# Performance work log

Hardware: AMD Instinct MI355X
Metric: run time of the kernel (lower is better)

## Reference

```python
import jax, jax.numpy as jnp
import numpy as np

DIM = 768
NUM_HEADS = 12
HEAD_DIM = DIM // NUM_HEADS
SCALE = HEAD_DIM ** -0.5


def setup_inputs() -> dict:
    key = jax.random.key(0)
    k1, k2, k3, k4 = jax.random.split(key, 4)
    x = jax.random.normal(k1, (4, 2048, DIM), dtype=jnp.float32)
    # Linear weights stored as [in, out] (torch stores [out, in]; math identical)
    w_qkv = jax.random.normal(k2, (DIM, 3 * DIM), dtype=jnp.float32) * (DIM ** -0.5)
    w_proj = jax.random.normal(k3, (DIM, DIM), dtype=jnp.float32) * (DIM ** -0.5)
    b_proj = jax.random.normal(k4, (DIM,), dtype=jnp.float32) * 0.02
    return {"x": x, "w_qkv": w_qkv, "w_proj": w_proj, "b_proj": b_proj}


def reference(x, w_qkv, w_proj, b_proj):
    b, n, d = x.shape
    qkv = x @ w_qkv  # [b, n, 3*d]
    # '(qkv h d)' layout: leading split is qkv, then heads, then head_dim
    qkv = qkv.reshape(b, n, 3, NUM_HEADS, HEAD_DIM).transpose(2, 0, 3, 1, 4)
    q, k, v = qkv[0], qkv[1], qkv[2]  # each [b, h, n, hd]
    alpha = jnp.einsum('bhqd,bhkd->bhqk', q, k) * SCALE  # [b, h, n, n]
    attn = jax.nn.softmax(alpha, axis=-1)
    out = jnp.einsum('bhqk,bhkd->bhqd', attn, v)  # [b, h, n, hd]
    out = out.transpose(0, 2, 1, 3).reshape(b, n, d)  # b n (h d)
    return out @ w_proj + b_proj
```

## Files before the change

### kernel.cpp

```cpp
#include <hip/hip_runtime.h>
#include <hip/hip_bf16.h>


typedef short s16x8 __attribute__((ext_vector_type(8)));
typedef short s16x4 __attribute__((ext_vector_type(4)));
typedef float f32x4 __attribute__((ext_vector_type(4)));
typedef float f32x16 __attribute__((ext_vector_type(16)));
typedef unsigned int u32;
typedef unsigned int u32x2 __attribute__((ext_vector_type(2)));
typedef unsigned int u32x4 __attribute__((ext_vector_type(4)));

#define NHEADS 12
#define HDIM   64
#define SEQ    2048
#define BATCH  4
#define DMODEL 768
#define MTOT   (BATCH*SEQ)
#define K3     (3*DMODEL)
#define QSCALE 0.18033688f

#define CAST_BLOCKS ((MTOT * DMODEL / 4) / 256)
#define TQ_BLOCKS   ((K3 / 64) * (DMODEL / 64))
#define TP_BLOCKS   ((DMODEL / 64) * (DMODEL / 64))

__device__ __forceinline__ short f2bf(float f) {
  return __builtin_bit_cast(short, __float2bfloat16(f));
}
__device__ __forceinline__ u32 pack2bf_rh(float lo, float hi) {
  u32 a = __builtin_bit_cast(u32, lo) + 0x8000u;
  u32 b = __builtin_bit_cast(u32, hi) + 0x8000u;
  return __builtin_amdgcn_perm(b, a, 0x07060302u);
}
__device__ __forceinline__ u32 pack2bf_tr(float lo, float hi) {
  return __builtin_amdgcn_perm(__builtin_bit_cast(u32, hi),
                               __builtin_bit_cast(u32, lo), 0x07060302u);
}
__device__ __forceinline__ f32x4 mfma16(s16x8 a, s16x8 b, f32x4 c) {
  return __builtin_amdgcn_mfma_f32_16x16x32_bf16(a, b, c, 0, 0, 0);
}
__device__ __forceinline__ f32x16 mfma32(s16x8 a, s16x8 b, f32x16 c) {
  return __builtin_amdgcn_mfma_f32_32x32x16_bf16(a, b, c, 0, 0, 0);
}
__device__ __forceinline__ void gload_lds16(const void* g, void* l) {
  __builtin_amdgcn_global_load_lds(
      (const __attribute__((address_space(1))) void*)g,
      (__attribute__((address_space(3))) void*)l, 16, 0, 0);
}

__global__ __launch_bounds__(256) void k_prep(const float* __restrict__ x,
                                              const float* __restrict__ w_qkv,
                                              const float* __restrict__ w_proj,
                                              short* __restrict__ Xb,
                                              short* __restrict__ WqkvT,
                                              short* __restrict__ WprojT) {
  __shared__ short t[64][74];
  const int bid = blockIdx.x, tid = threadIdx.x;

  if (bid < CAST_BLOCKS) {
    int i = bid * 256 + tid;
    float4 f = reinterpret_cast<const float4*>(x)[i];
    s16x4 v;
    v[0] = f2bf(f.x); v[1] = f2bf(f.y); v[2] = f2bf(f.z); v[3] = f2bf(f.w);
    reinterpret_cast<s16x4*>(Xb)[i] = v;
    return;
  }
  const float* in;
  short* out;
  int C, idx;
  if (bid < CAST_BLOCKS + TQ_BLOCKS) {
    in = w_qkv; out = WqkvT; C = K3; idx = bid - CAST_BLOCKS;
  } else {
    in = w_proj; out = WprojT; C = DMODEL; idx = bid - CAST_BLOCKS - TQ_BLOCKS;
  }
  const int c0 = (idx % (C / 64)) * 64;
  const int r0 = (idx / (C / 64)) * 64;
  {
    const int r = tid >> 2, j0 = (tid & 3) * 16;
    const float* ip = in + (size_t)(r0 + r) * C + c0 + j0;
#pragma unroll
    for (int k = 0; k < 16; k += 4) {
      float4 f = *reinterpret_cast<const float4*>(ip + k);
      t[r][j0 + k + 0] = f2bf(f.x); t[r][j0 + k + 1] = f2bf(f.y);
      t[r][j0 + k + 2] = f2bf(f.z); t[r][j0 + k + 3] = f2bf(f.w);
    }
  }
  __syncthreads();
  {
    const int c = tid >> 2, rr0 = (tid & 3) * 16;
    short* op = out + (size_t)(c0 + c) * DMODEL + r0 + rr0;
#pragma unroll
    for (int k = 0; k < 16; k += 8) {
      s16x8 v;
#pragma unroll
      for (int q = 0; q < 8; ++q) v[q] = t[rr0 + k + q][c];
      *reinterpret_cast<s16x8*>(op + k) = v;
    }
  }
}

__global__ __launch_bounds__(512, 4) void k_gemm_qkv(const short* __restrict__ Xb,
                                                     const short* __restrict__ WT,
                                                     short* __restrict__ Qb,
                                                     short* __restrict__ Kb,
                                                     short* __restrict__ Vt) {
  __shared__ short As[2][64 * 64];
  __shared__ short Bs[2][128 * 64];
  const int tid = threadIdx.x;
  const int orig = blockIdx.x;
  const int wg = (orig & 7) * (2304 / 8) + (orig >> 3);
  const int n0 = (wg % 18) * 128, m0 = (wg / 18) * 64;
  const int lane = tid & 63, w = tid >> 6;
  const int wr = w >> 2, wc = w & 3;
  const int g = lane >> 4, r16 = lane & 15;

  const int srow = tid >> 3;
  const int scc  = (tid & 7) ^ (srow & 7);
  const short* gaA = Xb + (size_t)(m0 + srow) * DMODEL + scc * 8;
  const short* gaB = WT + (size_t)(n0 + srow) * DMODEL + scc * 8;
  short* lA = &As[0][0] + w * 512;
  short* lB = &Bs[0][0] + w * 512;

#define GSTAGE(b, k0)                                                          \
  { gload_lds16(gaA + (k0),                         lA + (b) * 4096);          \
    gload_lds16(gaB + (k0),                         lB + (b) * 8192);          \
    gload_lds16(gaB + (size_t)64 * DMODEL + (k0),   lB + (b) * 8192 + 4096); }

  f32x4 acc[2][2] = {};
  const int key = (r16 & 7) << 4;

  GSTAGE(0, 0)
  for (int t = 0; t < DMODEL / 64; ++t) {
    const int b = t & 1;
    if (t + 1 < DMODEL / 64) {
      GSTAGE(b ^ 1, (t + 1) * 64)
      asm volatile("s_waitcnt vmcnt(3)" ::: "memory");
    } else {
      asm volatile("s_waitcnt vmcnt(0)" ::: "memory");
    }
    __builtin_amdgcn_s_barrier();
    __builtin_amdgcn_sched_barrier(0);

    const char* Ab = (const char*)&As[0][0] + b * 8192;
    const char* Bb = (const char*)&Bs[0][0] + b * 16384;
    s16x8 a[2][2], bf[2][2];
#pragma unroll
    for (int i = 0; i < 2; ++i)
#pragma unroll
      for (int kk = 0; kk < 2; ++kk)
        a[i][kk] = *(const s16x8*)(Ab + (((wr * 32 + i * 16 + r16) * 128 + kk * 64 + g * 16) ^ key));
#pragma unroll
    for (int j = 0; j < 2; ++j)
#pragma unroll
      for (int kk = 0; kk < 2; ++kk)
        bf[j][kk] = *(const s16x8*)(Bb + (((wc * 32 + j * 16 + r16) * 128 + kk * 64 + g * 16) ^ key));
#pragma unroll
    for (int kk = 0; kk < 2; ++kk)
#pragma unroll
      for (int i = 0; i < 2; ++i)
#pragma unroll
        for (int j = 0; j < 2; ++j)
          acc[i][j] = mfma16(a[i][kk], bf[j][kk], acc[i][j]);

    __builtin_amdgcn_sched_barrier(0);
    __builtin_amdgcn_s_barrier();
  }
#undef GSTAGE

#pragma unroll
  for (int i = 0; i < 2; ++i) {
#pragma unroll
    for (int jn = 0; jn < 2; ++jn) {
      const int c = n0 + wc * 32 + jn * 16 + r16;
#pragma unroll
      for (int rr = 0; rr < 4; ++rr) {
        const int m = m0 + wr * 32 + i * 16 + g * 4 + rr;
        const float a = acc[i][jn][rr];
        const int bb = m >> 11, ns = m & 2047;
        if (c < DMODEL) {
          const int h = c >> 6, d = c & 63;
          Qb[((bb * NHEADS + h) * SEQ + ns) * HDIM + d] = f2bf(a * QSCALE);
        } else if (c < 2 * DMODEL) {
          const int cc = c - DMODEL, h = cc >> 6, d = cc & 63;
          Kb[((bb * NHEADS + h) * SEQ + ns) * HDIM + d] = f2bf(a);
        } else {
          const int cc = c - 2 * DMODEL, h = cc >> 6, d = cc & 63;
          Vt[((bb * NHEADS + h) * HDIM + d) * SEQ + ns] = f2bf(a);
        }
      }
    }
  }
}

__global__ __launch_bounds__(256, 3) void k_attn(const short* __restrict__ Qb,
                                                 const short* __restrict__ Kb,
                                                 const short* __restrict__ Vtg,
                                                 short* __restrict__ Ctx) {
  __shared__ short Kt[3][64 * 64];
  __shared__ short Vt[3][64 * 64];

  const int tid = threadIdx.x, lane = tid & 63, w = tid >> 6;
  const int l31 = lane & 31, hi = lane >> 5;

  const int orig = blockIdx.y * gridDim.x + blockIdx.x;
  const int wg = (orig & 7) * (768 / 8) + (orig >> 3);
  const int qx = wg & 15;
  const int bh = wg >> 4;
  const int bb = bh / NHEADS, h = bh - bb * NHEADS;
  const int q0w = qx * 128 + w * 32;

  const short* Qp = Qb + (size_t)bh * SEQ * HDIM;
  const short* Kp = Kb + (size_t)bh * SEQ * HDIM;
  const short* Vp = Vtg + (size_t)bh * HDIM * SEQ;
  const int key4 = (lane & 7) << 4;

  const int sr1 = tid >> 3, sr2 = 32 + sr1;
  const int c1 = (tid & 7) ^ (sr1 & 7);
  const int c2 = (tid & 7) ^ (sr2 & 7);
  const short* kg1 = Kp + sr1 * HDIM + c1 * 8;
  const short* kg2 = Kp + sr2 * HDIM + c2 * 8;
  const short* vg1 = Vp + (size_t)sr1 * SEQ + c1 * 8;
  const short* vg2 = Vp + (size_t)sr2 * SEQ + c2 * 8;
  short* kld = &Kt[0][0] + w * 512;
  short* vld = &Vt[0][0] + w * 512;

#define STAGE(b, kb)                                                           \
  { gload_lds16(kg1 + (size_t)(kb) * HDIM, kld + (b) * 4096);                  \
    gload_lds16(kg2 + (size_t)(kb) * HDIM, kld + (b) * 4096 + 2048);           \
    gload_lds16(vg1 + (kb),                vld + (b) * 4096);                  \
    gload_lds16(vg2 + (kb),                vld + (b) * 4096 + 2048); }

  s16x8 aq[4];
#pragma unroll
  for (int kk = 0; kk < 4; ++kk)
    aq[kk] = *reinterpret_cast<const s16x8*>(&Qp[(q0w + l31) * HDIM + kk * 16 + hi * 8]);

  float sacc = 0.f;
  f32x16 accO[2] = {};

  STAGE(0, 0)
  int cur = 0, nxt = 1;

  for (int t = 0; t < SEQ / 64; ++t) {
    if (t + 1 < SEQ / 64) {
      STAGE(nxt, (t + 1) * 64)
      asm volatile("s_waitcnt vmcnt(4)" ::: "memory");
    } else {
      asm volatile("s_waitcnt vmcnt(0)" ::: "memory");
    }
    __builtin_amdgcn_s_barrier();
    __builtin_amdgcn_sched_barrier(0);

    const char* Kc = (const char*)Kt[cur];
    const char* Vc = (const char*)Vt[cur];

    f32x16 s0 = {}, s1 = {};
    __builtin_amdgcn_s_setprio(1);
#pragma unroll
    for (int kk = 0; kk < 4; ++kk) {
      const int cb = kk * 32 + hi * 16;
      s16x8 k0_ = *(const s16x8*)(Kc + (((l31)      * 128 + cb) ^ key4));
      s16x8 k1_ = *(const s16x8*)(Kc + (((l31 + 32) * 128 + cb) ^ key4));
      s0 = mfma32(k0_, aq[kk], s0);
      s1 = mfma32(k1_, aq[kk], s1);
    }
    __builtin_amdgcn_s_setprio(0);

    u32 A0[8], A1[8];
    float rs0 = 0.f, rs1 = 0.f, rs2 = 0.f, rs3 = 0.f;
#pragma unroll
    for (int r2 = 0; r2 < 8; ++r2) {
      float pa = __builtin_amdgcn_exp2f(s0[2 * r2]);
      float pb = __builtin_amdgcn_exp2f(s0[2 * r2 + 1]);
      rs0 += pa; rs1 += pb;
      A0[r2] = pack2bf_tr(pa, pb);
      float pc = __builtin_amdgcn_exp2f(s1[2 * r2]);
      float pd = __builtin_amdgcn_exp2f(s1[2 * r2 + 1]);
      rs2 += pc; rs3 += pd;
      A1[r2] = pack2bf_tr(pc, pd);
    }
    sacc += (rs0 + rs1) + (rs2 + rs3);

    __builtin_amdgcn_s_setprio(1);
#define PVW(Akg, KGOFF, S)                                                     \
    { u32 F0 = Akg[4 * (S)],     F2 = Akg[4 * (S) + 2];                        \
      u32 F1 = Akg[4 * (S) + 1], F3 = Akg[4 * (S) + 3];                        \
      asm volatile("v_permlane32_swap_b32 %0, %1" : "+v"(F0), "+v"(F2));       \
      asm volatile("v_permlane32_swap_b32 %0, %1" : "+v"(F1), "+v"(F3));       \
      u32x4 uv; uv[0] = F0; uv[1] = F1; uv[2] = F2; uv[3] = F3;                \
      s16x8 pfrag = __builtin_bit_cast(s16x8, uv);                             \
      const int cb_ = (KGOFF) + (S) * 32 + hi * 16;                            \
      s16x8 v0_ = *(const s16x8*)(Vc + (((l31)      * 128 + cb_) ^ key4));     \
      s16x8 v1_ = *(const s16x8*)(Vc + (((l31 + 32) * 128 + cb_) ^ key4));     \
      accO[0] = mfma32(v0_, pfrag, accO[0]);                                   \
      accO[1] = mfma32(v1_, pfrag, accO[1]); }
    PVW(A0, 0, 0) PVW(A0, 0, 1) PVW(A1, 64, 0) PVW(A1, 64, 1)
#undef PVW
    __builtin_amdgcn_s_setprio(0);

    cur = nxt;
    nxt = (nxt + 1 == 3) ? 0 : nxt + 1;
  }
#undef STAGE

  sacc += __shfl_xor(sacc, 32);
  const float inv = 1.0f / sacc;
  short* rowp = Ctx + (size_t)(bb * SEQ + q0w + l31) * DMODEL + h * HDIM + 4 * hi;
#pragma unroll
  for (int dt = 0; dt < 2; ++dt) {
#pragma unroll
    for (int rq = 0; rq < 4; ++rq) {
      u32x2 ov;
      ov[0] = pack2bf_rh(accO[dt][rq * 4 + 0] * inv, accO[dt][rq * 4 + 1] * inv);
      ov[1] = pack2bf_rh(accO[dt][rq * 4 + 2] * inv, accO[dt][rq * 4 + 3] * inv);
      *reinterpret_cast<u32x2*>(rowp + dt * 32 + rq * 8) = ov;
    }
  }
}

__global__ __launch_bounds__(512, 4) void k_gemm_proj(const short* __restrict__ Ctx,
                                                      const short* __restrict__ WT,
                                                      const float* __restrict__ bias,
                                                      float* __restrict__ Out) {
  __shared__ short As[2][64 * 64];
  __shared__ short Bs[2][128 * 64];
  const int tid = threadIdx.x;
  const int orig = blockIdx.x;
  const int wg = (orig & 7) * (768 / 8) + (orig >> 3);
  const int n0 = (wg % 6) * 128, m0 = (wg / 6) * 64;
  const int lane = tid & 63, w = tid >> 6;
  const int wr = w >> 2, wc = w & 3;
  const int g = lane >> 4, r16 = lane & 15;

  const int srow = tid >> 3;
  const int scc  = (tid & 7) ^ (srow & 7);
  const short* gaA = Ctx + (size_t)(m0 + srow) * DMODEL + scc * 8;
  const short* gaB = WT + (size_t)(n0 + srow) * DMODEL + scc * 8;
  short* lA = &As[0][0] + w * 512;
  short* lB = &Bs[0][0] + w * 512;

#define GSTAGE(b, k0)                                                          \
  { gload_lds16(gaA + (k0),                         lA + (b) * 4096);          \
    gload_lds16(gaB + (k0),                         lB + (b) * 8192);          \
    gload_lds16(gaB + (size_t)64 * DMODEL + (k0),   lB + (b) * 8192 + 4096); }

  f32x4 acc[2][2] = {};
  const int key = (r16 & 7) << 4;

  GSTAGE(0, 0)
  for (int t = 0; t < DMODEL / 64; ++t) {
    const int b = t & 1;
    if (t + 1 < DMODEL / 64) {
      GSTAGE(b ^ 1, (t + 1) * 64)
      asm volatile("s_waitcnt vmcnt(3)" ::: "memory");
    } else {
      asm volatile("s_waitcnt vmcnt(0)" ::: "memory");
    }
    __builtin_amdgcn_s_barrier();
    __builtin_amdgcn_sched_barrier(0);

    const char* Ab = (const char*)&As[0][0] + b * 8192;
    const char* Bb = (const char*)&Bs[0][0] + b * 16384;
    s16x8 a[2][2], bf[2][2];
#pragma unroll
    for (int i = 0; i < 2; ++i)
#pragma unroll
      for (int kk = 0; kk < 2; ++kk)
        a[i][kk] = *(const s16x8*)(Ab + (((wr * 32 + i * 16 + r16) * 128 + kk * 64 + g * 16) ^ key));
#pragma unroll
    for (int j = 0; j < 2; ++j)
#pragma unroll
      for (int kk = 0; kk < 2; ++kk)
        bf[j][kk] = *(const s16x8*)(Bb + (((wc * 32 + j * 16 + r16) * 128 + kk * 64 + g * 16) ^ key));
#pragma unroll
    for (int kk = 0; kk < 2; ++kk)
#pragma unroll
      for (int i = 0; i < 2; ++i)
#pragma unroll
        for (int j = 0; j < 2; ++j)
          acc[i][j] = mfma16(a[i][kk], bf[j][kk], acc[i][j]);

    __builtin_amdgcn_sched_barrier(0);
    __builtin_amdgcn_s_barrier();
  }
#undef GSTAGE

#pragma unroll
  for (int i = 0; i < 2; ++i) {
#pragma unroll
    for (int jn = 0; jn < 2; ++jn) {
      const int c = n0 + wc * 32 + jn * 16 + r16;
      const float bv = bias[c];
#pragma unroll
      for (int rr = 0; rr < 4; ++rr) {
        const int m = m0 + wr * 32 + i * 16 + g * 4 + rr;
        Out[(size_t)m * DMODEL + c] = acc[i][jn][rr] + bv;
      }
    }
  }
}

extern "C" void kernel_launch(void* const* d_in, const int* in_sizes, int n_in,
                              void* d_out, int out_size, void* d_ws, size_t ws_size,
                              hipStream_t stream) {
  const float* x      = (const float*)d_in[0];
  const float* w_qkv  = (const float*)d_in[1];
  const float* w_proj = (const float*)d_in[2];
  const float* b_proj = (const float*)d_in[3];
  float* out = (float*)d_out;

  char* ws = (char*)d_ws;
  const size_t SZ_X = (size_t)MTOT * DMODEL * 2;
  short* Xb     = (short*)ws;                 ws += SZ_X;
  short* WqkvT  = (short*)ws;                 ws += (size_t)K3 * DMODEL * 2;
  short* WprojT = (short*)ws;                 ws += (size_t)DMODEL * DMODEL * 2;
  short* Qb     = (short*)ws;                 ws += SZ_X;
  short* Kb     = (short*)ws;                 ws += SZ_X;
  short* Vt     = (short*)ws;                 ws += SZ_X;
  short* Ctxb   = Xb;

  k_prep<<<CAST_BLOCKS + TQ_BLOCKS + TP_BLOCKS, 256, 0, stream>>>(
      x, w_qkv, w_proj, Xb, WqkvT, WprojT);

  k_gemm_qkv<<<2304, 512, 0, stream>>>(Xb, WqkvT, Qb, Kb, Vt);
  k_attn<<<dim3(SEQ / 128, BATCH * NHEADS), 256, 0, stream>>>(Qb, Kb, Vt, Ctxb);
  k_gemm_proj<<<768, 512, 0, stream>>>(Ctxb, WprojT, b_proj, out);
}
```

Baseline: 153.7 us.

## Double-buffer attention LDS with compile-time offsets and MFMA row-sum

```diff
diff --git a/kernel.cpp b/kernel.cpp
--- a/kernel.cpp
+++ b/kernel.cpp
@@ -195,8 +195,7 @@
                                                  const short* __restrict__ Kb,
                                                  const short* __restrict__ Vtg,
                                                  short* __restrict__ Ctx) {
-  __shared__ short Kt[3][64 * 64];
-  __shared__ short Vt[3][64 * 64];
+  __shared__ short LDSB[4 * 64 * 64];
 
   const int tid = threadIdx.x, lane = tid & 63, w = tid >> 6;
   const int l31 = lane & 31, hi = lane >> 5;
@@ -220,8 +219,8 @@
   const short* kg2 = Kp + sr2 * HDIM + c2 * 8;
   const short* vg1 = Vp + (size_t)sr1 * SEQ + c1 * 8;
   const short* vg2 = Vp + (size_t)sr2 * SEQ + c2 * 8;
-  short* kld = &Kt[0][0] + w * 512;
-  short* vld = &Vt[0][0] + w * 512;
+  short* kld = LDSB + w * 512;
+  short* vld = LDSB + 8192 + w * 512;
 
 #define STAGE(b, kb)                                                           \
   { gload_lds16(kg1 + (size_t)(kb) * HDIM, kld + (b) * 4096);                  \
@@ -234,76 +233,77 @@
   for (int kk = 0; kk < 4; ++kk)
     aq[kk] = *reinterpret_cast<const s16x8*>(&Qp[(q0w + l31) * HDIM + kk * 16 + hi * 8]);
 
-  float sacc = 0.f;
+  s16x8 ones;
+#pragma unroll
+  for (int i = 0; i < 8; ++i) ones[i] = (short)0x3F80;
+
+  int addrA[4];
+#pragma unroll
+  for (int i = 0; i < 4; ++i) addrA[i] = l31 * 128 + ((i * 32 + hi * 16) ^ key4);
+  const char* lb = (const char*)LDSB;
+
+  f32x16 saccv = {};
   f32x16 accO[2] = {};
 
-  STAGE(0, 0)
-  int cur = 0, nxt = 1;
-
-  for (int t = 0; t < SEQ / 64; ++t) {
-    if (t + 1 < SEQ / 64) {
-      STAGE(nxt, (t + 1) * 64)
-      asm volatile("s_waitcnt vmcnt(4)" ::: "memory");
-    } else {
-      asm volatile("s_waitcnt vmcnt(0)" ::: "memory");
-    }
-    __builtin_amdgcn_s_barrier();
-    __builtin_amdgcn_sched_barrier(0);
-
-    const char* Kc = (const char*)Kt[cur];
-    const char* Vc = (const char*)Vt[cur];
-
-    f32x16 s0 = {}, s1 = {};
-    __builtin_amdgcn_s_setprio(1);
-#pragma unroll
-    for (int kk = 0; kk < 4; ++kk) {
-      const int cb = kk * 32 + hi * 16;
-      s16x8 k0_ = *(const s16x8*)(Kc + (((l31)      * 128 + cb) ^ key4));
-      s16x8 k1_ = *(const s16x8*)(Kc + (((l31 + 32) * 128 + cb) ^ key4));
-      s0 = mfma32(k0_, aq[kk], s0);
-      s1 = mfma32(k1_, aq[kk], s1);
-    }
-    __builtin_amdgcn_s_setprio(0);
-
-    u32 A0[8], A1[8];
-    float rs0 = 0.f, rs1 = 0.f, rs2 = 0.f, rs3 = 0.f;
-#pragma unroll
-    for (int r2 = 0; r2 < 8; ++r2) {
-      float pa = __builtin_amdgcn_exp2f(s0[2 * r2]);
-      float pb = __builtin_amdgcn_exp2f(s0[2 * r2 + 1]);
-      rs0 += pa; rs1 += pb;
-      A0[r2] = pack2bf_tr(pa, pb);
-      float pc = __builtin_amdgcn_exp2f(s1[2 * r2]);
-      float pd = __builtin_amdgcn_exp2f(s1[2 * r2 + 1]);
-      rs2 += pc; rs3 += pd;
-      A1[r2] = pack2bf_tr(pc, pd);
-    }
-    sacc += (rs0 + rs1) + (rs2 + rs3);
-
-    __builtin_amdgcn_s_setprio(1);
-#define PVW(Akg, KGOFF, S)                                                     \
-    { u32 F0 = Akg[4 * (S)],     F2 = Akg[4 * (S) + 2];                        \
-      u32 F1 = Akg[4 * (S) + 1], F3 = Akg[4 * (S) + 3];                        \
+#define PVW(Akg, I, b)                                                         \
+    { u32 F0 = Akg[4 * ((I) & 1)],     F2 = Akg[4 * ((I) & 1) + 2];            \
+      u32 F1 = Akg[4 * ((I) & 1) + 1], F3 = Akg[4 * ((I) & 1) + 3];            \
       asm volatile("v_permlane32_swap_b32 %0, %1" : "+v"(F0), "+v"(F2));       \
       asm volatile("v_permlane32_swap_b32 %0, %1" : "+v"(F1), "+v"(F3));       \
       u32x4 uv; uv[0] = F0; uv[1] = F1; uv[2] = F2; uv[3] = F3;                \
       s16x8 pfrag = __builtin_bit_cast(s16x8, uv);                             \
-      const int cb_ = (KGOFF) + (S) * 32 + hi * 16;                            \
-      s16x8 v0_ = *(const s16x8*)(Vc + (((l31)      * 128 + cb_) ^ key4));     \
-      s16x8 v1_ = *(const s16x8*)(Vc + (((l31 + 32) * 128 + cb_) ^ key4));     \
+      s16x8 v0_ = *(const s16x8*)(lb + 16384 + (b) * 8192 + addrA[I]);         \
+      s16x8 v1_ = *(const s16x8*)(lb + 16384 + (b) * 8192 + 4096 + addrA[I]);  \
+      saccv = mfma32(ones, pfrag, saccv);                                      \
       accO[0] = mfma32(v0_, pfrag, accO[0]);                                   \
       accO[1] = mfma32(v1_, pfrag, accO[1]); }
-    PVW(A0, 0, 0) PVW(A0, 0, 1) PVW(A1, 64, 0) PVW(A1, 64, 1)
+
+#define ITER(b, t)                                                             \
+  {                                                                            \
+    if ((t) + 1 < SEQ / 64) {                                                  \
+      STAGE((b) ^ 1, ((t) + 1) * 64)                                           \
+      asm volatile("s_waitcnt vmcnt(4)" ::: "memory");                         \
+    } else {                                                                   \
+      asm volatile("s_waitcnt vmcnt(0)" ::: "memory");                         \
+    }                                                                          \
+    __builtin_amdgcn_s_barrier();                                              \
+    __builtin_amdgcn_sched_barrier(0);                                         \
+    f32x16 s0 = {}, s1 = {};                                                   \
+    __builtin_amdgcn_s_setprio(1);                                             \
+    _Pragma("unroll")                                                          \
+    for (int kk = 0; kk < 4; ++kk) {                                           \
+      s16x8 k0_ = *(const s16x8*)(lb + (b) * 8192 + addrA[kk]);                \
+      s16x8 k1_ = *(const s16x8*)(lb + (b) * 8192 + 4096 + addrA[kk]);         \
+      s0 = mfma32(k0_, aq[kk], s0);                                            \
+      s1 = mfma32(k1_, aq[kk], s1);                                            \
+    }                                                                          \
+    __builtin_amdgcn_s_setprio(0);                                             \
+    u32 A0[8], A1[8];                                                          \
+    _Pragma("unroll")                                                          \
+    for (int r2 = 0; r2 < 8; ++r2) {                                           \
+      A0[r2] = pack2bf_tr(__builtin_amdgcn_exp2f(s0[2 * r2]),                  \
+                          __builtin_amdgcn_exp2f(s0[2 * r2 + 1]));             \
+      A1[r2] = pack2bf_tr(__builtin_amdgcn_exp2f(s1[2 * r2]),                  \
+                          __builtin_amdgcn_exp2f(s1[2 * r2 + 1]));             \
+    }                                                                          \
+    __builtin_amdgcn_s_setprio(1);                                             \
+    PVW(A0, 0, b) PVW(A0, 1, b) PVW(A1, 2, b) PVW(A1, 3, b)                    \
+    __builtin_amdgcn_s_setprio(0);                                             \
+    __builtin_amdgcn_sched_barrier(0);                                         \
+    __builtin_amdgcn_s_barrier();                                              \
+  }
+
+  STAGE(0, 0)
+#pragma unroll 1
+  for (int t = 0; t < SEQ / 64; t += 2) {
+    ITER(0, t)
+    ITER(1, t + 1)
+  }
+#undef ITER
 #undef PVW
-    __builtin_amdgcn_s_setprio(0);
-
-    cur = nxt;
-    nxt = (nxt + 1 == 3) ? 0 : nxt + 1;
-  }
 #undef STAGE
 
-  sacc += __shfl_xor(sacc, 32);
-  const float inv = 1.0f / sacc;
+  const float inv = 1.0f / saccv[0];
   short* rowp = Ctx + (size_t)(bb * SEQ + q0w + l31) * DMODEL + h * HDIM + 4 * hi;
 #pragma unroll
   for (int dt = 0; dt < 2; ++dt) {
```

After: 153.1 us. No clear change (-0.4%).
